# Performance work log

Measured on AMD Instinct MI355X. Metric: run time of the kernel, lower is better.

Reference implementation:

```python
import jax, jax.numpy as jnp
import numpy as np

# cost weights from __init__
W_CLASS = 1.0
W_KPTS = 1.0
W_CTRS = 1.0
W_DELTAS = 1.0
W_KPTS_CLASS = 1.0


def setup_inputs() -> dict:
    key = jax.random.key(0)
    k1, k2, k3, k4 = jax.random.split(key, 4)
    bs, Q, C, P = 16, 300, 2, 320
    pred_logits = jax.random.normal(k1, (bs, Q, C), dtype=jnp.float32)
    pred_kpts = jax.random.uniform(k2, (bs, Q, 53), dtype=jnp.float32)
    tgt_kpts = jax.random.uniform(k3, (P, 54), dtype=jnp.float32)
    # all visibility flags == 1 so the `if all(tgt_kpts[:,2])` branch is taken
    tgt_kpts = tgt_kpts.at[:, 2::3].set(1.0)
    tgt_ids = jax.random.randint(k4, (P,), 0, C)
    return {"pred_logits": pred_logits, "pred_kpts": pred_kpts,
            "tgt_kpts": tgt_kpts, "tgt_ids": tgt_ids}


def _cost_matrix(pred_logits, pred_kpts, tgt_kpts, tgt_ids):
    bs, Q, C = pred_logits.shape
    N = bs * Q
    P = tgt_kpts.shape[0]

    out_prob = jax.nn.softmax(pred_logits.reshape(N, C), axis=-1)  # [N,C]
    out_k = pred_kpts.reshape(N, -1)                               # [N,53]

    cost_class = -out_prob[:, tgt_ids]                             # [N,P]

    out_kpts_ids = out_k[:, 4::3]                                  # [N,17]
    tgt_kpts_ids = tgt_kpts[:, 5::3]                               # [P,17]

    x = jnp.concatenate([out_k[:, 0:1], out_k[:, 2::3]], axis=1)   # [N,18]
    y = jnp.concatenate([out_k[:, 1:2], out_k[:, 3::3]], axis=1)   # [N,18]
    x_abs = jnp.concatenate([x[:, 0:1], (x[:, 1:] - 0.5) * 2.0 + x[:, 0:1]], axis=1)
    y_abs = jnp.concatenate([y[:, 0:1], (y[:, 1:] - 0.5) * 2.0 + y[:, 0:1]], axis=1)

    tgt_x = tgt_kpts[:, 0::3]                                      # [P,18]
    tgt_y = tgt_kpts[:, 1::3]                                      # [P,18]
    tgt_x_abs = jnp.concatenate([tgt_x[:, 0:1], (tgt_x[:, 1:] - 0.5) * 2.0 + tgt_x[:, 0:1]], axis=1)
    tgt_y_abs = jnp.concatenate([tgt_y[:, 0:1], (tgt_y[:, 1:] - 0.5) * 2.0 + tgt_y[:, 0:1]], axis=1)

    vis = (tgt_kpts[:, 2::3] == 1.0).astype(pred_kpts.dtype)       # [P,18]
    visT = vis.T                                                   # [18,P]

    def interleave_pred(xc, yc):
        # [N,18,P] masked per target, interleaved to [N,36,P]
        mx = xc[:, :, None] * visT[None, :, :]
        my = yc[:, :, None] * visT[None, :, :]
        return jnp.stack([mx, my], axis=2).reshape(N, 36, P)

    def interleave_tgt(xc, yc):
        return jnp.stack([xc * vis, yc * vis], axis=2).reshape(P, 36)

    ok = interleave_pred(x, y)                 # [N,36,P]
    tk = interleave_tgt(tgt_x, tgt_y)          # [P,36]
    ok_abs = interleave_pred(x_abs, y_abs)     # [N,36,P]
    tk_abs = interleave_tgt(tgt_x_abs, tgt_y_abs)

    # vectorized version of the per-person cdist loop
    cost_deltas = jnp.abs(ok[:, 2:, :] - tk.T[None, 2:, :]).sum(axis=1)          # L1, [N,P]
    cost_kpts = jnp.abs(ok_abs[:, 2:, :] - tk_abs.T[None, 2:, :]).sum(axis=1)    # L1, [N,P]
    cost_ctrs = jnp.sqrt(((ok[:, :2, :] - tk.T[None, :2, :]) ** 2).sum(axis=1))  # L2, [N,P]
    cost_kpts_class = jnp.sqrt(((out_kpts_ids[:, None, :] - tgt_kpts_ids[None, :, :]) ** 2).sum(-1))  # [N,P]

    Cmat = (W_KPTS * cost_kpts + W_CTRS * cost_ctrs + W_DELTAS * cost_deltas
            + W_CLASS * cost_class + W_KPTS_CLASS * cost_kpts_class)
    return Cmat.reshape(bs, Q, P)


def reference(pred_logits, pred_kpts, tgt_kpts, tgt_ids):
    return _cost_matrix(pred_logits, pred_kpts, tgt_kpts, tgt_ids)
```

## Files before the change

### kernel.cpp

```cpp
#include <hip/hip_runtime.h>
#include <math.h>

#define BS 16
#define QN 300
#define CN 2
#define PN 320
#define NN (BS * QN)
#define KPRED 53
#define KTGT 54
#define TILE_N 4

__global__ __launch_bounds__(PN) void hungarian_cost_kernel(
    const float* __restrict__ pred_logits,
    const float* __restrict__ pred_kpts,
    const float* __restrict__ tgt_kpts,
    const int*   __restrict__ tgt_ids,
    float* __restrict__ out)
{
    const int p  = threadIdx.x;
    const int n0 = blockIdx.x * TILE_N;

    float tx[18], ty[18], w[18];
    unsigned vmask = 0u;
    {
        const float* t = tgt_kpts + (size_t)p * KTGT;
        #pragma unroll
        for (int j = 0; j < 18; ++j) {
            tx[j] = t[3 * j];
            ty[j] = t[3 * j + 1];
            const float vv = t[3 * j + 2];
            w[j] = vv;
            vmask |= (vv == 1.0f) ? (1u << j) : 0u;
        }
    }
    const int cls = tgt_ids[p];

    float lg[2 * TILE_N];
    #pragma unroll
    for (int i = 0; i < 2 * TILE_N; ++i) lg[i] = pred_logits[n0 * CN + i];

    #pragma unroll
    for (int ni = 0; ni < TILE_N; ++ni) {
        const int n = n0 + ni;

        float k[KPRED];
        {
            const float* kp = pred_kpts + (size_t)n * KPRED;
            #pragma unroll
            for (int i = 0; i < KPRED; ++i) k[i] = kp[i];
        }

        const float dx0 = k[0] - tx[0];
        const float dy0 = k[1] - ty[0];

        float cd = 0.0f;
        float ck = 0.0f;
        float cq = 0.0f;
        #pragma unroll
        for (int j = 1; j < 18; ++j) {
            const float vj = (float)((vmask >> j) & 1u);
            const float dx = k[3 * j - 1] - tx[j];
            const float dy = k[3 * j]     - ty[j];
            cd = fmaf(vj, fabsf(dx) + fabsf(dy), cd);
            const float ax = fmaf(2.0f, dx, dx0);
            const float ay = fmaf(2.0f, dy, dy0);
            ck = fmaf(vj, fabsf(ax) + fabsf(ay), ck);
            const float d = k[3 * j + 1] - w[j];
            cq = fmaf(d, d, cq);
        }

        const float v0 = (float)(vmask & 1u);
        const float cc = v0 * sqrtf(fmaf(dx0, dx0, dy0 * dy0));

        const float l0 = lg[2 * ni], l1 = lg[2 * ni + 1];
        const float m  = fmaxf(l0, l1);
        const float e0 = __expf(l0 - m);
        const float e1 = __expf(l1 - m);
        const float inv = 1.0f / (e0 + e1);
        const float ccls = -((cls == 0) ? e0 : e1) * inv;

        out[(size_t)n * PN + p] = ck + cc + cd + ccls + sqrtf(cq);
    }
}

extern "C" void kernel_launch(void* const* d_in, const int* in_sizes, int n_in,
                              void* d_out, int out_size, void* d_ws, size_t ws_size,
                              hipStream_t stream) {
    const float* pred_logits = (const float*)d_in[0];
    const float* pred_kpts   = (const float*)d_in[1];
    const float* tgt_kpts    = (const float*)d_in[2];
    const int*   tgt_ids     = (const int*)d_in[3];
    float* out = (float*)d_out;

    dim3 grid(NN / TILE_N);
    dim3 block(PN);
    hipLaunchKernelGGL(hungarian_cost_kernel, grid, block, 0, stream,
                       pred_logits, pred_kpts, tgt_kpts, tgt_ids, out);
}
```

Measured before the change: 74.42 us.

## Remap threads to predictions with wave-uniform targets and LDS-staged output tile

Measured after the change: 77.49 us. +4.1%, slower.

```diff
diff --git a/kernel.cpp b/kernel.cpp
--- a/kernel.cpp
+++ b/kernel.cpp
@@ -8,78 +8,94 @@
 #define NN (BS * QN)
 #define KPRED 53
 #define KTGT 54
-#define TILE_N 4
 
-__global__ __launch_bounds__(PN) void hungarian_cost_kernel(
+#define NTILE 64
+#define PCH 32
+#define NWAVES 4
+#define PPW (PCH / NWAVES)
+#define TPAD 36
+
+__global__ __launch_bounds__(256) void hungarian_cost_kernel(
     const float* __restrict__ pred_logits,
     const float* __restrict__ pred_kpts,
     const float* __restrict__ tgt_kpts,
     const int*   __restrict__ tgt_ids,
     float* __restrict__ out)
 {
-    const int p  = threadIdx.x;
-    const int n0 = blockIdx.x * TILE_N;
+    __shared__ float sk[NTILE * KPRED];
+    __shared__ float sl[NTILE * CN];
+    __shared__ float tile[NTILE * TPAD];
 
-    float tx[18], ty[18], w[18];
-    unsigned vmask = 0u;
+    const int tid  = threadIdx.x;
+    const int lane = tid & 63;
+    const int wid  = __builtin_amdgcn_readfirstlane(tid >> 6);
+    const int n0 = blockIdx.x * NTILE;
+    const int p0 = blockIdx.y * PCH;
+
+    for (int i = tid; i < NTILE * KPRED; i += 256)
+        sk[i] = pred_kpts[(size_t)n0 * KPRED + i];
+    for (int i = tid; i < NTILE * CN; i += 256)
+        sl[i] = pred_logits[(size_t)n0 * CN + i];
+    __syncthreads();
+
+    float x[18], y[18], kc[17];
     {
-        const float* t = tgt_kpts + (size_t)p * KTGT;
+        const float* k = &sk[lane * KPRED];
+        x[0] = k[0]; y[0] = k[1];
         #pragma unroll
-        for (int j = 0; j < 18; ++j) {
-            tx[j] = t[3 * j];
-            ty[j] = t[3 * j + 1];
-            const float vv = t[3 * j + 2];
-            w[j] = vv;
-            vmask |= (vv == 1.0f) ? (1u << j) : 0u;
+        for (int j = 1; j < 18; ++j) {
+            x[j] = k[3 * j - 1];
+            y[j] = k[3 * j];
+            kc[j - 1] = k[3 * j + 1];
         }
     }
-    const int cls = tgt_ids[p];
+    const float l0 = sl[lane * 2], l1 = sl[lane * 2 + 1];
+    const float mm = fmaxf(l0, l1);
+    const float e0 = __expf(l0 - mm), e1 = __expf(l1 - mm);
+    const float inv = 1.0f / (e0 + e1);
+    const float pr0 = e0 * inv, pr1 = e1 * inv;
 
-    float lg[2 * TILE_N];
-    #pragma unroll
-    for (int i = 0; i < 2 * TILE_N; ++i) lg[i] = pred_logits[n0 * CN + i];
+    #pragma unroll 2
+    for (int it = 0; it < PPW; ++it) {
+        const int pc = wid * PPW + it;
+        const int p  = p0 + pc;
+        const float* t = tgt_kpts + (size_t)p * KTGT;
+        const int cls = tgt_ids[p];
 
-    #pragma unroll
-    for (int ni = 0; ni < TILE_N; ++ni) {
-        const int n = n0 + ni;
+        const float tx0 = t[0], ty0 = t[1];
+        const float v0  = (t[2] == 1.0f) ? 1.0f : 0.0f;
+        const float dx0 = x[0] - tx0;
+        const float dy0 = y[0] - ty0;
 
-        float k[KPRED];
-        {
-            const float* kp = pred_kpts + (size_t)n * KPRED;
-            #pragma unroll
-            for (int i = 0; i < KPRED; ++i) k[i] = kp[i];
-        }
-
-        const float dx0 = k[0] - tx[0];
-        const float dy0 = k[1] - ty[0];
-
-        float cd = 0.0f;
-        float ck = 0.0f;
-        float cq = 0.0f;
+        float cd = 0.0f, ck = 0.0f, cq = 0.0f;
         #pragma unroll
         for (int j = 1; j < 18; ++j) {
-            const float vj = (float)((vmask >> j) & 1u);
-            const float dx = k[3 * j - 1] - tx[j];
-            const float dy = k[3 * j]     - ty[j];
+            const float txj = t[3 * j], tyj = t[3 * j + 1], wj = t[3 * j + 2];
+            const float vj  = (wj == 1.0f) ? 1.0f : 0.0f;
+            const float dx = x[j] - txj;
+            const float dy = y[j] - tyj;
             cd = fmaf(vj, fabsf(dx) + fabsf(dy), cd);
             const float ax = fmaf(2.0f, dx, dx0);
             const float ay = fmaf(2.0f, dy, dy0);
             ck = fmaf(vj, fabsf(ax) + fabsf(ay), ck);
-            const float d = k[3 * j + 1] - w[j];
+            const float d = kc[j - 1] - wj;
             cq = fmaf(d, d, cq);
         }
 
-        const float v0 = (float)(vmask & 1u);
-        const float cc = v0 * sqrtf(fmaf(dx0, dx0, dy0 * dy0));
+        const float cc   = v0 * sqrtf(fmaf(dx0, dx0, dy0 * dy0));
+        const float ccls = -((cls == 0) ? pr0 : pr1);
 
-        const float l0 = lg[2 * ni], l1 = lg[2 * ni + 1];
-        const float m  = fmaxf(l0, l1);
-        const float e0 = __expf(l0 - m);
-        const float e1 = __expf(l1 - m);
-        const float inv = 1.0f / (e0 + e1);
-        const float ccls = -((cls == 0) ? e0 : e1) * inv;
+        tile[lane * TPAD + pc] = ck + cc + cd + ccls + sqrtf(cq);
+    }
+    __syncthreads();
 
-        out[(size_t)n * PN + p] = ck + cc + cd + ccls + sqrtf(cq);
+    {
+        const int r  = tid >> 2;
+        const int c0 = (tid & 3) * 8;
+        const float* src = &tile[r * TPAD + c0];
+        float* dst = &out[(size_t)(n0 + r) * PN + p0 + c0];
+        #pragma unroll
+        for (int i = 0; i < 8; ++i) dst[i] = src[i];
     }
 }
 
@@ -92,8 +108,8 @@
     const int*   tgt_ids     = (const int*)d_in[3];
     float* out = (float*)d_out;
 
-    dim3 grid(NN / TILE_N);
-    dim3 block(PN);
+    dim3 grid(NN / NTILE, PN / PCH);
+    dim3 block(NWAVES * 64);
     hipLaunchKernelGGL(hungarian_cost_kernel, grid, block, 0, stream,
                        pred_logits, pred_kpts, tgt_kpts, tgt_ids, out);
 }
```
